# Kernel optimization log

Hardware: AMD Instinct MI355X
Metric: run time of the kernel (lower is better)

Reference implementation:

```python
import jax, jax.numpy as jnp
import numpy as np


def _bilinear_sample(fea, x, y):
    # fea: [B,C,H,W]; x,y: [B,D,HW] pixel coords. grid_sample bilinear, zeros padding, align_corners=True
    B, C, H, W = fea.shape
    x0 = jnp.floor(x)
    y0 = jnp.floor(y)
    wx1 = x - x0
    wy1 = y - y0
    flat = fea.reshape(B, C, H * W)

    def corner(xi, yi, w):
        valid = (xi >= 0) & (xi <= W - 1) & (yi >= 0) & (yi <= H - 1)
        idx = jnp.clip(yi, 0, H - 1).astype(jnp.int32) * W + jnp.clip(xi, 0, W - 1).astype(jnp.int32)
        v = jnp.take_along_axis(flat[:, :, None, :], idx[:, None, :, :], axis=3)  # [B,C,D,HW]
        return v * (w * valid)[:, None]

    return (corner(x0, y0, (1 - wx1) * (1 - wy1)) + corner(x0 + 1, y0, wx1 * (1 - wy1))
            + corner(x0, y0 + 1, (1 - wx1) * wy1) + corner(x0 + 1, y0 + 1, wx1 * wy1))


def _build_proj(p):
    # p: [B,2,4,4] -> 4x4 with top 3x4 = K @ [R|t]
    top = jnp.einsum('bij,bjk->bik', p[:, 1, :3, :3], p[:, 0, :3, :4])
    return p[:, 0].at[:, :3, :4].set(top)


def _forward(depth_values, features, proj_matrices, depth_interval, view_weights, CostNum):
    V = features.shape[0]
    ref_fea = features[0]
    B, C, H, W = ref_fea.shape
    # inverse-depth range sampling (per-pixel, CasMVSNet-style)
    inv_d = 1.0 / depth_values[:, 0]                      # [B,H,W]
    itv = depth_interval[:, 0]                            # [B,H,W]
    low = inv_d - (CostNum / 2.0) * itv
    step = (CostNum * itv) / (CostNum - 1)                # (high-low)/(D-1)
    samp = low[:, None] + jnp.arange(CostNum, dtype=inv_d.dtype)[None, :, None, None] * step[:, None]
    depth = (1.0 / samp).reshape(B, CostNum, H * W)       # back to metric depth [B,D,HW]

    ref_inv = jnp.linalg.inv(_build_proj(proj_matrices[:, 0]))
    ys, xs = jnp.meshgrid(jnp.arange(H, dtype=inv_d.dtype), jnp.arange(W, dtype=inv_d.dtype), indexing='ij')
    xyz = jnp.stack([xs.ravel(), ys.ravel(), jnp.ones(H * W, dtype=inv_d.dtype)], 0)  # [3,HW]

    vol = jnp.zeros((B, 1, CostNum, H, W), inv_d.dtype)
    wsum = jnp.full((B, 1, 1, H, W), 1e-5, inv_d.dtype)
    for i in range(1, V):
        proj = jnp.einsum('bij,bjk->bik', _build_proj(proj_matrices[:, i]), ref_inv)
        rot_xyz = jnp.einsum('bij,jn->bin', proj[:, :3, :3], xyz)                     # [B,3,HW]
        pxyz = rot_xyz[:, :, None, :] * depth[:, None] + proj[:, :3, 3][:, :, None, None]
        gx = pxyz[:, 0] / pxyz[:, 2]
        gy = pxyz[:, 1] / pxyz[:, 2]
        warped = _bilinear_sample(features[i], gx, gy).reshape(B, C, CostNum, H, W)
        wv = (warped * ref_fea[:, :, None]).mean(axis=1, keepdims=True)               # [B,1,D,H,W]
        vw = view_weights[:, i - 1][:, None, None]                                    # [B,1,1,H,W]
        vol = vol + wv * vw
        wsum = wsum + vw
    sim = vol / wsum
    # torch broadcasts [B,1,D,H,W] into the [B,C,D,H,W] buffer -> all C channels equal
    return jnp.broadcast_to(sim, (B, C, CostNum, H, W)).reshape(B, C * CostNum, H, W)


def setup_inputs():
    key = jax.random.key(0)
    ks = jax.random.split(key, 4)
    V, B, C, H, W = 5, 2, 32, 256, 320
    features = jax.random.normal(ks[0], (V, B, C, H, W), jnp.float32)
    depth_values = jax.random.uniform(ks[1], (B, 1, H, W), jnp.float32, minval=0.5, maxval=2.0)
    depth_interval = jax.random.uniform(ks[2], (B, 1, H, W), jnp.float32, minval=0.01, maxval=0.03)
    view_weights = jax.random.uniform(ks[3], (B, V - 1, H, W), jnp.float32, minval=0.1, maxval=1.0)
    K = np.array([[300.0, 0.0, W / 2.0], [0.0, 300.0, H / 2.0], [0.0, 0.0, 1.0]], np.float32)
    proj = np.zeros((B, V, 2, 4, 4), np.float32)
    for v in range(V):
        E = np.eye(4, dtype=np.float32)
        E[0, 3] = 0.1 * v  # camera baseline along x
        proj[:, v, 0] = E
        proj[:, v, 1] = np.eye(4, dtype=np.float32)
        proj[:, v, 1, :3, :3] = K
    return {"depth_values": depth_values, "features": features, "proj_matrices": jnp.asarray(proj),
            "depth_interval": depth_interval, "depth_max": 100, "depth_min": 1, "CostNum": 4,
            "view_weights": view_weights}


def reference(depth_values, features, proj_matrices, depth_interval, depth_max, depth_min, CostNum, view_weights):
    # depth_max/depth_min are unused in the per-pixel sampling path of the original helper
    return _forward(depth_values, features, proj_matrices, depth_interval, view_weights, CostNum)
```

## Files before the change

kernel.cpp:

```cpp
#include <hip/hip_runtime.h>

static constexpr int V  = 5;
static constexpr int B  = 2;
static constexpr int C  = 32;
static constexpr int H  = 256;
static constexpr int W  = 320;
static constexpr int CN = 4;
static constexpr int HW = H * W;
static constexpr int CG = 8;
static constexpr int NG = 4;

__device__ __forceinline__ float2 ld2(const float* p) {
    float2 v;
    __builtin_memcpy(&v, p, sizeof(float2));
    return v;
}

__global__ void setup_proj_kernel(const float* __restrict__ pm, float* __restrict__ params) {
    int b = threadIdx.x;
    if (b >= B) return;

    float M[V][16];
    for (int v = 0; v < V; ++v) {
        const float* E  = pm + ((size_t)(b * V + v) * 2 + 0) * 16;
        const float* Km = pm + ((size_t)(b * V + v) * 2 + 1) * 16;
        for (int r = 0; r < 3; ++r)
            for (int c = 0; c < 4; ++c) {
                float s = 0.f;
                for (int k = 0; k < 3; ++k) s += Km[r * 4 + k] * E[k * 4 + c];
                M[v][r * 4 + c] = s;
            }
        for (int c = 0; c < 4; ++c) M[v][12 + c] = E[12 + c];
    }

    float A[9], bb[3];
    for (int r = 0; r < 3; ++r) {
        for (int c = 0; c < 3; ++c) A[r * 3 + c] = M[0][r * 4 + c];
        bb[r] = M[0][r * 4 + 3];
    }
    float det = A[0] * (A[4] * A[8] - A[5] * A[7])
              - A[1] * (A[3] * A[8] - A[5] * A[6])
              + A[2] * (A[3] * A[7] - A[4] * A[6]);
    float id = 1.f / det;
    float Ai[9];
    Ai[0] = (A[4] * A[8] - A[5] * A[7]) * id;
    Ai[1] = (A[2] * A[7] - A[1] * A[8]) * id;
    Ai[2] = (A[1] * A[5] - A[2] * A[4]) * id;
    Ai[3] = (A[5] * A[6] - A[3] * A[8]) * id;
    Ai[4] = (A[0] * A[8] - A[2] * A[6]) * id;
    Ai[5] = (A[2] * A[3] - A[0] * A[5]) * id;
    Ai[6] = (A[3] * A[7] - A[4] * A[6]) * id;
    Ai[7] = (A[1] * A[6] - A[0] * A[7]) * id;
    Ai[8] = (A[0] * A[4] - A[1] * A[3]) * id;
    float bi[3];
    for (int r = 0; r < 3; ++r)
        bi[r] = -(Ai[r * 3 + 0] * bb[0] + Ai[r * 3 + 1] * bb[1] + Ai[r * 3 + 2] * bb[2]);

    float Minv[16];
    for (int r = 0; r < 3; ++r) {
        for (int c = 0; c < 3; ++c) Minv[r * 4 + c] = Ai[r * 3 + c];
        Minv[r * 4 + 3] = bi[r];
    }
    Minv[12] = 0.f; Minv[13] = 0.f; Minv[14] = 0.f; Minv[15] = 1.f;

    for (int v = 1; v < V; ++v) {
        float* dst = params + (size_t)(b * (V - 1) + (v - 1)) * 12;
        for (int r = 0; r < 3; ++r)
            for (int c = 0; c < 4; ++c) {
                float s = 0.f;
                for (int k = 0; k < 4; ++k) s += M[v][r * 4 + k] * Minv[k * 4 + c];
                dst[r * 4 + c] = s;
            }
    }
}

__global__ __launch_bounds__(256) void getcost_kernel(
    const float* __restrict__ depth_values,
    const float* __restrict__ features,
    const float* __restrict__ depth_interval,
    const float* __restrict__ view_weights,
    const float* __restrict__ params,
    float* __restrict__ out)
{
    const int tid = threadIdx.x;
    const int p   = tid & 63;
    const int g   = tid >> 6;
    const int x   = blockIdx.x * 64 + p;
    const int y   = blockIdx.y;
    const int b   = blockIdx.z;
    const int pix = y * W + x;

    __shared__ float sp[(V - 1) * 12];
    __shared__ float sred[NG][CN][64];
    if (tid < (V - 1) * 12) sp[tid] = params[b * (V - 1) * 12 + tid];
    __syncthreads();

    const float invd = 1.f / depth_values[(size_t)b * HW + pix];
    const float itv  = depth_interval[(size_t)b * HW + pix];
    const float low  = invd - (CN * 0.5f) * itv;
    const float step = (CN * itv) / (float)(CN - 1);
    float dep[CN];
#pragma unroll
    for (int k = 0; k < CN; ++k) dep[k] = 1.f / (low + (float)k * step);

    const float* refp = features + ((size_t)b * C + g * CG) * HW + pix;
    float rf[CG];
#pragma unroll
    for (int c = 0; c < CG; ++c) rf[c] = __builtin_nontemporal_load(refp + (size_t)c * HW);

    float vol[CN] = {0.f, 0.f, 0.f, 0.f};
    float wsum = 1e-5f;

    const float fx = (float)x, fy = (float)y;

    for (int i = 1; i < V; ++i) {
        const float* P = sp + (i - 1) * 12;
        const float rx = P[0] * fx + P[1] * fy + P[2];
        const float ry = P[4] * fx + P[5] * fy + P[6];
        const float rz = P[8] * fx + P[9] * fy + P[10];
        const float tx = P[3], ty = P[7], tz = P[11];

        const float* src = features + ((size_t)(i * B + b) * C + g * CG) * HW;
        const float vw = view_weights[((size_t)b * (V - 1) + (i - 1)) * HW + pix];
        const float scale = vw * (1.f / (float)C);

        int   ib0[CN], ib1[CN];
        float wA0[CN], wB0[CN], wA1[CN], wB1[CN];
#pragma unroll
        for (int k = 0; k < CN; ++k) {
            const float d  = dep[k];
            const float px = rx * d + tx;
            const float py = ry * d + ty;
            const float pz = rz * d + tz;
            const float iz = 1.f / pz;
            const float gx = px * iz;
            const float gy = py * iz;

            const float x0f = floorf(gx), y0f = floorf(gy);
            const float wx1 = gx - x0f, wy1 = gy - y0f;
            const float wx0 = 1.f - wx1, wy0 = 1.f - wy1;
            const int x0 = (int)x0f, y0 = (int)y0f;
            const int x1 = x0 + 1, y1 = y0 + 1;

            const bool vx0 = (x0 >= 0) && (x0 <= W - 1);
            const bool vx1 = (x1 >= 0) && (x1 <= W - 1);
            const bool vy0 = (y0 >= 0) && (y0 <= H - 1);
            const bool vy1 = (y1 >= 0) && (y1 <= H - 1);

            const int cy0 = min(max(y0, 0), H - 1);
            const int cy1 = min(max(y1, 0), H - 1);
            const int bx  = min(max(x0, 0), W - 2);
            const int s   = x0 - bx;

            const float w00 = wx0 * wy0 * ((vx0 && vy0) ? scale : 0.f);
            const float w10 = wx1 * wy0 * ((vx1 && vy0) ? scale : 0.f);
            const float w01 = wx0 * wy1 * ((vx0 && vy1) ? scale : 0.f);
            const float w11 = wx1 * wy1 * ((vx1 && vy1) ? scale : 0.f);

            wA0[k] = (s == 0) ? w00 : ((s == -1) ? w10 : 0.f);
            wB0[k] = (s == 0) ? w10 : ((s == 1) ? w00 : 0.f);
            wA1[k] = (s == 0) ? w01 : ((s == -1) ? w11 : 0.f);
            wB1[k] = (s == 0) ? w11 : ((s == 1) ? w01 : 0.f);

            ib0[k] = cy0 * W + bx;
            ib1[k] = cy1 * W + bx;
        }

#pragma unroll
        for (int c = 0; c < CG; ++c) {
            const float* fc = src + (size_t)c * HW;
            const float rfc = rf[c];
#pragma unroll
            for (int k = 0; k < CN; ++k) {
                const float2 p0 = ld2(fc + ib0[k]);
                const float2 p1 = ld2(fc + ib1[k]);
                float t = wA0[k] * p0.x;
                t = fmaf(wB0[k], p0.y, t);
                t = fmaf(wA1[k], p1.x, t);
                t = fmaf(wB1[k], p1.y, t);
                vol[k] = fmaf(rfc, t, vol[k]);
            }
        }
        wsum += vw;
    }

#pragma unroll
    for (int k = 0; k < CN; ++k) sred[g][k][p] = vol[k];
    __syncthreads();

    if (g == 0) {
        const float iws = 1.f / wsum;
#pragma unroll
        for (int k = 0; k < CN; ++k) {
            float s = sred[0][k][p] + sred[1][k][p] + sred[2][k][p] + sred[3][k][p];
            sred[0][k][p] = s * iws;
        }
    }
    __syncthreads();

    float* op = out + (size_t)b * C * CN * HW + pix;
#pragma unroll
    for (int jj = 0; jj < 32; ++jj) {
        const int j = g * 32 + jj;
        __builtin_nontemporal_store(sred[0][j & 3][p], op + (size_t)j * HW);
    }
}

extern "C" void kernel_launch(void* const* d_in, const int* in_sizes, int n_in,
                              void* d_out, int out_size, void* d_ws, size_t ws_size,
                              hipStream_t stream) {
    const float* depth_values   = (const float*)d_in[0];
    const float* features       = (const float*)d_in[1];
    const float* proj_matrices  = (const float*)d_in[2];
    const float* depth_interval = (const float*)d_in[3];
    const float* view_weights   = (const float*)d_in[7];
    float* out = (float*)d_out;
    float* params = (float*)d_ws;

    setup_proj_kernel<<<1, B, 0, stream>>>(proj_matrices, params);

    dim3 block(256, 1, 1);
    dim3 grid(W / 64, H, B);
    getcost_kernel<<<grid, block, 0, stream>>>(depth_values, features, depth_interval,
                                               view_weights, params, out);
}
```

Baseline: 301.5 us.

## Split source views across blocks and add separate finalize kernel for reduction and output

The per-view loop moves out of the main kernel: each block now handles one (batch, source view) pair, giving four times as many blocks, and writes per-view partial similarities to a workspace buffer. A new finalize kernel sums the partials, normalizes by the view-weight sum and writes the replicated output with vectorized nontemporal stores. Launch bounds add an occupancy hint and the block index is remapped so neighbouring blocks share a tile across views. In exchange the reference features and depths are reloaded per view, there is an extra kernel launch, and the partial buffer makes an extra round trip through memory.

```diff
diff --git a/kernel.cpp b/kernel.cpp
--- a/kernel.cpp
+++ b/kernel.cpp
@@ -9,10 +9,16 @@
 static constexpr int HW = H * W;
 static constexpr int CG = 8;
 static constexpr int NG = 4;
-
-__device__ __forceinline__ float2 ld2(const float* p) {
-    float2 v;
-    __builtin_memcpy(&v, p, sizeof(float2));
+static constexpr int XT = W / 64;
+
+static constexpr size_t PARTIAL_FLOATS = (size_t)B * (V - 1) * CN * HW;
+static constexpr size_t PARAMS_OFF     = PARTIAL_FLOATS;
+
+typedef float f32x2 __attribute__((ext_vector_type(2)));
+
+__device__ __forceinline__ f32x2 ld2(const float* p) {
+    f32x2 v;
+    __builtin_memcpy(&v, p, sizeof(f32x2));
     return v;
 }
 
@@ -74,25 +80,32 @@
     }
 }
 
-__global__ __launch_bounds__(256) void getcost_kernel(
+__global__ __launch_bounds__(256, 4) void partial_kernel(
     const float* __restrict__ depth_values,
     const float* __restrict__ features,
     const float* __restrict__ depth_interval,
     const float* __restrict__ view_weights,
     const float* __restrict__ params,
-    float* __restrict__ out)
+    float* __restrict__ partial)
 {
     const int tid = threadIdx.x;
     const int p   = tid & 63;
     const int g   = tid >> 6;
-    const int x   = blockIdx.x * 64 + p;
-    const int y   = blockIdx.y;
-    const int b   = blockIdx.z;
+
+    const int lid = blockIdx.x + XT * (blockIdx.y + H * blockIdx.z);
+    const int r   = lid & 7;
+    const int q   = lid >> 3;
+    const int b   = r >> 2;
+    const int iv  = r & 3;
+    const int xt  = q % XT;
+    const int y   = q / XT;
+
+    const int x   = xt * 64 + p;
     const int pix = y * W + x;
 
-    __shared__ float sp[(V - 1) * 12];
+    __shared__ float sp[12];
     __shared__ float sred[NG][CN][64];
-    if (tid < (V - 1) * 12) sp[tid] = params[b * (V - 1) * 12 + tid];
+    if (tid < 12) sp[tid] = params[(size_t)(b * (V - 1) + iv) * 12 + tid];
     __syncthreads();
 
     const float invd = 1.f / depth_values[(size_t)b * HW + pix];
@@ -108,80 +121,73 @@
 #pragma unroll
     for (int c = 0; c < CG; ++c) rf[c] = __builtin_nontemporal_load(refp + (size_t)c * HW);
 
+    const float fx = (float)x, fy = (float)y;
+    const float rx = sp[0] * fx + sp[1] * fy + sp[2];
+    const float ry = sp[4] * fx + sp[5] * fy + sp[6];
+    const float rz = sp[8] * fx + sp[9] * fy + sp[10];
+    const float tx = sp[3], ty = sp[7], tz = sp[11];
+
+    const float* src = features + ((size_t)((iv + 1) * B + b) * C + g * CG) * HW;
+    const float vw = view_weights[((size_t)b * (V - 1) + iv) * HW + pix];
+    const float scale = vw * (1.f / (float)C);
+
+    int   ib0[CN], ib1[CN];
+    float wA0[CN], wB0[CN], wA1[CN], wB1[CN];
+#pragma unroll
+    for (int k = 0; k < CN; ++k) {
+        const float d  = dep[k];
+        const float px = rx * d + tx;
+        const float py = ry * d + ty;
+        const float pz = rz * d + tz;
+        const float iz = 1.f / pz;
+        const float gx = px * iz;
+        const float gy = py * iz;
+
+        const float x0f = floorf(gx), y0f = floorf(gy);
+        const float wx1 = gx - x0f, wy1 = gy - y0f;
+        const float wx0 = 1.f - wx1, wy0 = 1.f - wy1;
+        const int x0 = (int)x0f, y0 = (int)y0f;
+        const int x1 = x0 + 1, y1 = y0 + 1;
+
+        const bool vx0 = (x0 >= 0) && (x0 <= W - 1);
+        const bool vx1 = (x1 >= 0) && (x1 <= W - 1);
+        const bool vy0 = (y0 >= 0) && (y0 <= H - 1);
+        const bool vy1 = (y1 >= 0) && (y1 <= H - 1);
+
+        const int cy0 = min(max(y0, 0), H - 1);
+        const int cy1 = min(max(y1, 0), H - 1);
+        const int bx  = min(max(x0, 0), W - 2);
+        const int s   = x0 - bx;
+
+        const float w00 = wx0 * wy0 * ((vx0 && vy0) ? scale : 0.f);
+        const float w10 = wx1 * wy0 * ((vx1 && vy0) ? scale : 0.f);
+        const float w01 = wx0 * wy1 * ((vx0 && vy1) ? scale : 0.f);
+        const float w11 = wx1 * wy1 * ((vx1 && vy1) ? scale : 0.f);
+
+        wA0[k] = (s == 0) ? w00 : ((s == -1) ? w10 : 0.f);
+        wB0[k] = (s == 0) ? w10 : ((s == 1) ? w00 : 0.f);
+        wA1[k] = (s == 0) ? w01 : ((s == -1) ? w11 : 0.f);
+        wB1[k] = (s == 0) ? w11 : ((s == 1) ? w01 : 0.f);
+
+        ib0[k] = cy0 * W + bx;
+        ib1[k] = cy1 * W + bx;
+    }
+
     float vol[CN] = {0.f, 0.f, 0.f, 0.f};
-    float wsum = 1e-5f;
-
-    const float fx = (float)x, fy = (float)y;
-
-    for (int i = 1; i < V; ++i) {
-        const float* P = sp + (i - 1) * 12;
-        const float rx = P[0] * fx + P[1] * fy + P[2];
-        const float ry = P[4] * fx + P[5] * fy + P[6];
-        const float rz = P[8] * fx + P[9] * fy + P[10];
-        const float tx = P[3], ty = P[7], tz = P[11];
-
-        const float* src = features + ((size_t)(i * B + b) * C + g * CG) * HW;
-        const float vw = view_weights[((size_t)b * (V - 1) + (i - 1)) * HW + pix];
-        const float scale = vw * (1.f / (float)C);
-
-        int   ib0[CN], ib1[CN];
-        float wA0[CN], wB0[CN], wA1[CN], wB1[CN];
+#pragma unroll
+    for (int c = 0; c < CG; ++c) {
+        const float* fc = src + (size_t)c * HW;
+        const float rfc = rf[c];
 #pragma unroll
         for (int k = 0; k < CN; ++k) {
-            const float d  = dep[k];
-            const float px = rx * d + tx;
-            const float py = ry * d + ty;
-            const float pz = rz * d + tz;
-            const float iz = 1.f / pz;
-            const float gx = px * iz;
-            const float gy = py * iz;
-
-            const float x0f = floorf(gx), y0f = floorf(gy);
-            const float wx1 = gx - x0f, wy1 = gy - y0f;
-            const float wx0 = 1.f - wx1, wy0 = 1.f - wy1;
-            const int x0 = (int)x0f, y0 = (int)y0f;
-            const int x1 = x0 + 1, y1 = y0 + 1;
-
-            const bool vx0 = (x0 >= 0) && (x0 <= W - 1);
-            const bool vx1 = (x1 >= 0) && (x1 <= W - 1);
-            const bool vy0 = (y0 >= 0) && (y0 <= H - 1);
-            const bool vy1 = (y1 >= 0) && (y1 <= H - 1);
-
-            const int cy0 = min(max(y0, 0), H - 1);
-            const int cy1 = min(max(y1, 0), H - 1);
-            const int bx  = min(max(x0, 0), W - 2);
-            const int s   = x0 - bx;
-
-            const float w00 = wx0 * wy0 * ((vx0 && vy0) ? scale : 0.f);
-            const float w10 = wx1 * wy0 * ((vx1 && vy0) ? scale : 0.f);
-            const float w01 = wx0 * wy1 * ((vx0 && vy1) ? scale : 0.f);
-            const float w11 = wx1 * wy1 * ((vx1 && vy1) ? scale : 0.f);
-
-            wA0[k] = (s == 0) ? w00 : ((s == -1) ? w10 : 0.f);
-            wB0[k] = (s == 0) ? w10 : ((s == 1) ? w00 : 0.f);
-            wA1[k] = (s == 0) ? w01 : ((s == -1) ? w11 : 0.f);
-            wB1[k] = (s == 0) ? w11 : ((s == 1) ? w01 : 0.f);
-
-            ib0[k] = cy0 * W + bx;
-            ib1[k] = cy1 * W + bx;
+            const f32x2 p0 = ld2(fc + ib0[k]);
+            const f32x2 p1 = ld2(fc + ib1[k]);
+            float t = wA0[k] * p0.x;
+            t = fmaf(wB0[k], p0.y, t);
+            t = fmaf(wA1[k], p1.x, t);
+            t = fmaf(wB1[k], p1.y, t);
+            vol[k] = fmaf(rfc, t, vol[k]);
         }
-
-#pragma unroll
-        for (int c = 0; c < CG; ++c) {
-            const float* fc = src + (size_t)c * HW;
-            const float rfc = rf[c];
-#pragma unroll
-            for (int k = 0; k < CN; ++k) {
-                const float2 p0 = ld2(fc + ib0[k]);
-                const float2 p1 = ld2(fc + ib1[k]);
-                float t = wA0[k] * p0.x;
-                t = fmaf(wB0[k], p0.y, t);
-                t = fmaf(wA1[k], p1.x, t);
-                t = fmaf(wB1[k], p1.y, t);
-                vol[k] = fmaf(rfc, t, vol[k]);
-            }
-        }
-        wsum += vw;
     }
 
 #pragma unroll
@@ -189,21 +195,52 @@
     __syncthreads();
 
     if (g == 0) {
-        const float iws = 1.f / wsum;
+        float* dst = partial + ((size_t)(b * (V - 1) + iv) * CN) * HW + pix;
 #pragma unroll
         for (int k = 0; k < CN; ++k) {
             float s = sred[0][k][p] + sred[1][k][p] + sred[2][k][p] + sred[3][k][p];
-            sred[0][k][p] = s * iws;
+            __builtin_nontemporal_store(s, dst + (size_t)k * HW);
         }
     }
-    __syncthreads();
+}
+
+__global__ __launch_bounds__(256) void finalize_kernel(
+    const float* __restrict__ partial,
+    const float* __restrict__ view_weights,
+    float* __restrict__ out)
+{
+    const int t   = blockIdx.x * 256 + threadIdx.x;
+    const int idx = t * 2;
+    const int b   = idx / HW;
+    const int pix = idx - b * HW;
+
+    float wsx = 1e-5f, wsy = 1e-5f;
+#pragma unroll
+    for (int i = 0; i < V - 1; ++i) {
+        f32x2 vw = ld2(view_weights + ((size_t)b * (V - 1) + i) * HW + pix);
+        wsx += vw.x; wsy += vw.y;
+    }
+    const float iwx = 1.f / wsx, iwy = 1.f / wsy;
+
+    f32x2 sim[CN];
+#pragma unroll
+    for (int k = 0; k < CN; ++k) {
+        float sx = 0.f, sy = 0.f;
+#pragma unroll
+        for (int i = 0; i < V - 1; ++i) {
+            f32x2 pv = ld2(partial + ((size_t)(b * (V - 1) + i) * CN + k) * HW + pix);
+            sx += pv.x; sy += pv.y;
+        }
+        sim[k].x = sx * iwx;
+        sim[k].y = sy * iwy;
+    }
 
     float* op = out + (size_t)b * C * CN * HW + pix;
 #pragma unroll
-    for (int jj = 0; jj < 32; ++jj) {
-        const int j = g * 32 + jj;
-        __builtin_nontemporal_store(sred[0][j & 3][p], op + (size_t)j * HW);
-    }
+    for (int c = 0; c < C; ++c)
+#pragma unroll
+        for (int k = 0; k < CN; ++k)
+            __builtin_nontemporal_store(sim[k], (f32x2*)(op + (size_t)(c * CN + k) * HW));
 }
 
 extern "C" void kernel_launch(void* const* d_in, const int* in_sizes, int n_in,
@@ -214,13 +251,15 @@
     const float* proj_matrices  = (const float*)d_in[2];
     const float* depth_interval = (const float*)d_in[3];
     const float* view_weights   = (const float*)d_in[7];
-    float* out = (float*)d_out;
-    float* params = (float*)d_ws;
+    float* out     = (float*)d_out;
+    float* partial = (float*)d_ws;
+    float* params  = (float*)d_ws + PARAMS_OFF;
 
     setup_proj_kernel<<<1, B, 0, stream>>>(proj_matrices, params);
 
-    dim3 block(256, 1, 1);
-    dim3 grid(W / 64, H, B);
-    getcost_kernel<<<grid, block, 0, stream>>>(depth_values, features, depth_interval,
-                                               view_weights, params, out);
-}
+    dim3 grid1(XT, H, B * (V - 1));
+    partial_kernel<<<grid1, 256, 0, stream>>>(depth_values, features, depth_interval,
+                                              view_weights, params, partial);
+
+    finalize_kernel<<<B * HW / 512, 256, 0, stream>>>(partial, view_weights, out);
+}
```

Result: no change. 299.0 us (-0.8%).
